# Optimization experiments

Measured on AMD Instinct MI355X. Metric: run time of the kernel, lower is better.

The kernel has to match this reference:

```python
import jax, jax.numpy as jnp
import numpy as np

SCALE = 2
GROUPS = 4
IN_CH = 256


def _init_pos(scale, groups):
    # torch: arange((-s+1)/2, (s-1)/2 + 1) / s
    h = (np.arange(scale) - (scale - 1) / 2.0) / scale
    hh, ww = np.meshgrid(h, h, indexing='ij')          # (s,s) each
    t = np.stack([hh, ww]).transpose(0, 2, 1)          # (2,s,s), transpose(1,2)
    rep = np.tile(t, (1, groups, 1))                   # (2, g*s, s)
    return jnp.asarray(rep.reshape(1, -1, 1, 1), dtype=jnp.float32)  # (1, 2*g*s^2, 1, 1)


def _pixel_shuffle(x, r):
    B, C, H, W = x.shape
    Co = C // (r * r)
    x = x.reshape(B, Co, r, r, H, W)
    x = x.transpose(0, 1, 4, 2, 5, 3)                  # (B,Co,H,r,W,r)
    return x.reshape(B, Co, H * r, W * r)


def _grid_sample_border(x, grid):
    # x: (N,C,H,W), grid: (N,Ho,Wo,2) in [-1,1], align_corners=False, border padding
    N, C, H, W = x.shape
    gx, gy = grid[..., 0], grid[..., 1]
    ix = jnp.clip(((gx + 1.0) * W - 1.0) * 0.5, 0.0, W - 1.0)
    iy = jnp.clip(((gy + 1.0) * H - 1.0) * 0.5, 0.0, H - 1.0)
    ix0 = jnp.floor(ix)
    iy0 = jnp.floor(iy)
    wx = (ix - ix0)[..., None]
    wy = (iy - iy0)[..., None]
    x0 = ix0.astype(jnp.int32)
    y0 = iy0.astype(jnp.int32)
    x1 = jnp.minimum(x0 + 1, W - 1)
    y1 = jnp.minimum(y0 + 1, H - 1)
    xt = x.transpose(0, 2, 3, 1)                       # NHWC for channel-last gather
    b = jnp.arange(N)[:, None, None]
    v00 = xt[b, y0, x0]
    v01 = xt[b, y0, x1]
    v10 = xt[b, y1, x0]
    v11 = xt[b, y1, x1]
    out = (v00 * (1 - wy) * (1 - wx) + v01 * (1 - wy) * wx
           + v10 * wy * (1 - wx) + v11 * wy * wx)      # (N,Ho,Wo,C)
    return out.transpose(0, 3, 1, 2)


def setup_inputs() -> dict:
    key = jax.random.key(0)
    k1, k2 = jax.random.split(key)
    B, C, H, W = 8, IN_CH, 80, 80
    out_ch = 2 * GROUPS * SCALE ** 2
    x = jax.random.normal(k1, (B, C, H, W), dtype=jnp.float32)
    w_off = jax.random.normal(k2, (out_ch, C, 1, 1), dtype=jnp.float32) * 0.001
    b_off = jnp.zeros((out_ch,), dtype=jnp.float32)
    return {"x": x, "w_off": w_off, "b_off": b_off}


def reference(x, w_off, b_off):
    B, C, H, W = x.shape
    s, g = SCALE, GROUPS
    # 1x1 conv predicting offsets
    off = jnp.einsum('bchw,oc->bohw', x, w_off[:, :, 0, 0]) + b_off[None, :, None, None]
    offset = off * 0.25 + _init_pos(s, g)              # (B, 2*g*s^2, H, W)
    offset = offset.reshape(B, 2, g * s * s, H, W)
    # pixel-center base coords: channel 0 = x (w), channel 1 = y (h)
    cx = jnp.arange(W, dtype=x.dtype) + 0.5
    cy = jnp.arange(H, dtype=x.dtype) + 0.5
    coords = jnp.stack([jnp.broadcast_to(cx[None, :], (H, W)),
                        jnp.broadcast_to(cy[:, None], (H, W))])   # (2,H,W)
    coords = coords[None, :, None]                     # (1,2,1,H,W)
    norm = jnp.array([W, H], dtype=x.dtype).reshape(1, 2, 1, 1, 1)
    coords = 2.0 * (coords + offset) / norm - 1.0      # (B,2,g*s^2,H,W)
    coords = coords.reshape(B, 2 * g * s * s, H, W)
    coords = _pixel_shuffle(coords, s)                 # (B, 2*g, s*H, s*W)
    coords = coords.reshape(B, 2, g, s * H, s * W)
    coords = coords.transpose(0, 2, 3, 4, 1).reshape(B * g, s * H, s * W, 2)
    xr = x.reshape(B * g, C // g, H, W)
    out = _grid_sample_border(xr, coords)              # (B*g, C/g, sH, sW)
    return out.reshape(B, C, s * H, s * W)
```

## Files before the change

kernel.cpp:

```cpp
#include <hip/hip_runtime.h>

#define W_IN 80
#define H_IN 80
#define HW_IN (W_IN * H_IN)
#define C_IN 256
#define NG 4
#define NOFF 32
#define W_OUT 160
#define H_OUT 160
#define HW_OUT (W_OUT * H_OUT)

__global__ __launch_bounds__(256) void conv_coords_kernel(
    const float* __restrict__ x, const float* __restrict__ w,
    const float* __restrict__ bias, float2* __restrict__ coords) {
  __shared__ float ws[C_IN * NOFF];
  const int t = threadIdx.x;
#pragma unroll
  for (int i = 0; i < (C_IN * NOFF) / 256; ++i) {
    int idx = i * 256 + t;
    int c = idx >> 5, o = idx & 31;
    ws[idx] = w[o * C_IN + c];
  }
  __syncthreads();

  const int p = blockIdx.x * 256 + t;
  const int b = p / HW_IN;
  const int yx = p - b * HW_IN;
  const float* xp = x + (size_t)b * C_IN * HW_IN + yx;

  float acc[NOFF];
#pragma unroll
  for (int o = 0; o < NOFF; ++o) acc[o] = bias[o];

#pragma unroll 4
  for (int c = 0; c < C_IN; ++c) {
    float v = xp[(size_t)c * HW_IN];
    const float4* w4 = reinterpret_cast<const float4*>(&ws[c * NOFF]);
#pragma unroll
    for (int o4 = 0; o4 < NOFF / 4; ++o4) {
      float4 wv = w4[o4];
      acc[o4 * 4 + 0] = fmaf(v, wv.x, acc[o4 * 4 + 0]);
      acc[o4 * 4 + 1] = fmaf(v, wv.y, acc[o4 * 4 + 1]);
      acc[o4 * 4 + 2] = fmaf(v, wv.z, acc[o4 * 4 + 2]);
      acc[o4 * 4 + 3] = fmaf(v, wv.w, acc[o4 * 4 + 3]);
    }
  }

  const int y = yx / W_IN;
  const int xc = yx - y * W_IN;
#pragma unroll
  for (int k = 0; k < 16; ++k) {
    float hx = (k & 1) ? 0.25f : -0.25f;
    float hy = (k & 2) ? 0.25f : -0.25f;
    float ix = fminf(fmaxf((float)xc + fmaf(0.25f, acc[k], hx), 0.0f),
                     (float)(W_IN - 1));
    float iy = fminf(fmaxf((float)y + fmaf(0.25f, acc[16 + k], hy), 0.0f),
                     (float)(H_IN - 1));
    coords[(size_t)(b * 16 + k) * HW_IN + yx] = make_float2(ix, iy);
  }
}

__global__ __launch_bounds__(256) void sample_kernel(
    const float* __restrict__ x, const float2* __restrict__ coords,
    float* __restrict__ out) {
  const int idx = blockIdx.x * 256 + threadIdx.x;
  const int ox = idx % W_OUT;
  const int r1d = idx / W_OUT;
  const int oy = r1d % H_OUT;
  const int r2d = r1d / H_OUT;
  const int gi = r2d & 3;
  const int b = r2d >> 2;

  const int xs = ox >> 1, j = ox & 1;
  const int ys = oy >> 1, i = oy & 1;
  const int k = gi * 4 + i * 2 + j;

  const float2 c2 = coords[(size_t)(b * 16 + k) * HW_IN + ys * W_IN + xs];
  const float fx0 = floorf(c2.x), fy0 = floorf(c2.y);
  const int x0 = (int)fx0, y0 = (int)fy0;
  const float wx = c2.x - fx0, wy = c2.y - fy0;
  const int x1 = min(x0 + 1, W_IN - 1), y1 = min(y0 + 1, H_IN - 1);

  const float w00 = (1.0f - wy) * (1.0f - wx);
  const float w01 = (1.0f - wy) * wx;
  const float w10 = wy * (1.0f - wx);
  const float w11 = wy * wx;

  const int o00 = y0 * W_IN + x0;
  const int o01 = y0 * W_IN + x1;
  const int o10 = y1 * W_IN + x0;
  const int o11 = y1 * W_IN + x1;

  const float* xp = x + (size_t)(b * C_IN + gi * 64) * HW_IN;
  float* op = out + (size_t)(b * C_IN + gi * 64) * HW_OUT + oy * W_OUT + ox;

#pragma unroll 4
  for (int c = 0; c < 64; ++c) {
    const float* pc = xp + c * HW_IN;
    float v = pc[o00] * w00 + pc[o01] * w01 + pc[o10] * w10 + pc[o11] * w11;
    op[c * HW_OUT] = v;
  }
}

extern "C" void kernel_launch(void* const* d_in, const int* in_sizes, int n_in,
                              void* d_out, int out_size, void* d_ws,
                              size_t ws_size, hipStream_t stream) {
  const float* x = (const float*)d_in[0];
  const float* w_off = (const float*)d_in[1];
  const float* b_off = (const float*)d_in[2];
  float* out = (float*)d_out;
  float2* coords = (float2*)d_ws;

  conv_coords_kernel<<<200, 256, 0, stream>>>(x, w_off, b_off, coords);
  sample_kernel<<<3200, 256, 0, stream>>>(x, coords, out);
}
```

Before: 329.2 us.

## Split conv channel reduction across waves and vectorize bilinear gathers

```diff
diff --git a/kernel.cpp b/kernel.cpp
--- a/kernel.cpp
+++ b/kernel.cpp
@@ -2,19 +2,24 @@
 
 #define W_IN 80
 #define H_IN 80
-#define HW_IN (W_IN * H_IN)
+#define HW_IN 6400
 #define C_IN 256
-#define NG 4
 #define NOFF 32
 #define W_OUT 160
 #define H_OUT 160
-#define HW_OUT (W_OUT * H_OUT)
+#define HW_OUT 25600
+
+typedef float f2u __attribute__((ext_vector_type(2), aligned(4)));
 
 __global__ __launch_bounds__(256) void conv_coords_kernel(
     const float* __restrict__ x, const float* __restrict__ w,
     const float* __restrict__ bias, float2* __restrict__ coords) {
   __shared__ float ws[C_IN * NOFF];
+  __shared__ float offb[64][NOFF + 1];
   const int t = threadIdx.x;
+  const int lane = t & 63;
+  const int wv = t >> 6;
+
 #pragma unroll
   for (int i = 0; i < (C_IN * NOFF) / 256; ++i) {
     int idx = i * 256 + t;
@@ -23,40 +28,70 @@
   }
   __syncthreads();
 
-  const int p = blockIdx.x * 256 + t;
-  const int b = p / HW_IN;
-  const int yx = p - b * HW_IN;
-  const float* xp = x + (size_t)b * C_IN * HW_IN + yx;
+  const int pix0 = blockIdx.x * 64;
+  const int b = blockIdx.x / 100;
+  const int yx0 = pix0 - b * HW_IN;
+  const int yx = yx0 + lane;
+
+  const float* xp = x + ((size_t)b * C_IN + wv * 64) * HW_IN + yx;
 
   float acc[NOFF];
 #pragma unroll
-  for (int o = 0; o < NOFF; ++o) acc[o] = bias[o];
+  for (int o = 0; o < NOFF; ++o) acc[o] = 0.0f;
 
 #pragma unroll 4
-  for (int c = 0; c < C_IN; ++c) {
-    float v = xp[(size_t)c * HW_IN];
-    const float4* w4 = reinterpret_cast<const float4*>(&ws[c * NOFF]);
+  for (int cc = 0; cc < 64; ++cc) {
+    float v = xp[(size_t)cc * HW_IN];
+    const float4* w4 = reinterpret_cast<const float4*>(&ws[(wv * 64 + cc) * NOFF]);
 #pragma unroll
     for (int o4 = 0; o4 < NOFF / 4; ++o4) {
-      float4 wv = w4[o4];
-      acc[o4 * 4 + 0] = fmaf(v, wv.x, acc[o4 * 4 + 0]);
-      acc[o4 * 4 + 1] = fmaf(v, wv.y, acc[o4 * 4 + 1]);
-      acc[o4 * 4 + 2] = fmaf(v, wv.z, acc[o4 * 4 + 2]);
-      acc[o4 * 4 + 3] = fmaf(v, wv.w, acc[o4 * 4 + 3]);
+      float4 wvv = w4[o4];
+      acc[o4 * 4 + 0] = fmaf(v, wvv.x, acc[o4 * 4 + 0]);
+      acc[o4 * 4 + 1] = fmaf(v, wvv.y, acc[o4 * 4 + 1]);
+      acc[o4 * 4 + 2] = fmaf(v, wvv.z, acc[o4 * 4 + 2]);
+      acc[o4 * 4 + 3] = fmaf(v, wvv.w, acc[o4 * 4 + 3]);
     }
   }
 
-  const int y = yx / W_IN;
-  const int xc = yx - y * W_IN;
+  __syncthreads();
+  if (wv == 0) {
 #pragma unroll
-  for (int k = 0; k < 16; ++k) {
+    for (int o = 0; o < NOFF; ++o) offb[lane][o] = acc[o] + bias[o];
+  }
+  __syncthreads();
+  if (wv == 1) {
+#pragma unroll
+    for (int o = 0; o < NOFF; ++o) offb[lane][o] += acc[o];
+  }
+  __syncthreads();
+  if (wv == 2) {
+#pragma unroll
+    for (int o = 0; o < NOFF; ++o) offb[lane][o] += acc[o];
+  }
+  __syncthreads();
+  if (wv == 3) {
+#pragma unroll
+    for (int o = 0; o < NOFF; ++o) offb[lane][o] += acc[o];
+  }
+  __syncthreads();
+
+#pragma unroll
+  for (int r = 0; r < 4; ++r) {
+    int id = r * 256 + t;
+    int k = id >> 6;
+    int px = id & 63;
+    float offx = offb[px][k];
+    float offy = offb[px][16 + k];
+    int yxp = yx0 + px;
+    int y = yxp / W_IN;
+    int xc = yxp - y * W_IN;
     float hx = (k & 1) ? 0.25f : -0.25f;
     float hy = (k & 2) ? 0.25f : -0.25f;
-    float ix = fminf(fmaxf((float)xc + fmaf(0.25f, acc[k], hx), 0.0f),
+    float ix = fminf(fmaxf((float)xc + fmaf(0.25f, offx, hx), 0.0f),
                      (float)(W_IN - 1));
-    float iy = fminf(fmaxf((float)y + fmaf(0.25f, acc[16 + k], hy), 0.0f),
+    float iy = fminf(fmaxf((float)y + fmaf(0.25f, offy, hy), 0.0f),
                      (float)(H_IN - 1));
-    coords[(size_t)(b * 16 + k) * HW_IN + yx] = make_float2(ix, iy);
+    coords[((size_t)b * 16 + k) * HW_IN + yxp] = make_float2(ix, iy);
   }
 }
 
@@ -65,40 +100,41 @@
     float* __restrict__ out) {
   const int idx = blockIdx.x * 256 + threadIdx.x;
   const int ox = idx % W_OUT;
-  const int r1d = idx / W_OUT;
-  const int oy = r1d % H_OUT;
-  const int r2d = r1d / H_OUT;
-  const int gi = r2d & 3;
-  const int b = r2d >> 2;
+  const int r1 = idx / W_OUT;
+  const int oy = r1 % H_OUT;
+  const int r2 = r1 / H_OUT;
+  const int gi = r2 & 3;
+  const int b = r2 >> 2;
 
   const int xs = ox >> 1, j = ox & 1;
   const int ys = oy >> 1, i = oy & 1;
   const int k = gi * 4 + i * 2 + j;
 
-  const float2 c2 = coords[(size_t)(b * 16 + k) * HW_IN + ys * W_IN + xs];
+  const float2 c2 = coords[((size_t)b * 16 + k) * HW_IN + ys * W_IN + xs];
   const float fx0 = floorf(c2.x), fy0 = floorf(c2.y);
   const int x0 = (int)fx0, y0 = (int)fy0;
   const float wx = c2.x - fx0, wy = c2.y - fy0;
-  const int x1 = min(x0 + 1, W_IN - 1), y1 = min(y0 + 1, H_IN - 1);
+  const int y1 = min(y0 + 1, H_IN - 1);
+  const int xl = min(x0, W_IN - 2);
+  const bool xe = (x0 == W_IN - 1);
 
-  const float w00 = (1.0f - wy) * (1.0f - wx);
-  const float w01 = (1.0f - wy) * wx;
-  const float w10 = wy * (1.0f - wx);
-  const float w11 = wy * wx;
+  const int o0 = y0 * W_IN + xl;
+  const int o1 = y1 * W_IN + xl;
 
-  const int o00 = y0 * W_IN + x0;
-  const int o01 = y0 * W_IN + x1;
-  const int o10 = y1 * W_IN + x0;
-  const int o11 = y1 * W_IN + x1;
-
-  const float* xp = x + (size_t)(b * C_IN + gi * 64) * HW_IN;
-  float* op = out + (size_t)(b * C_IN + gi * 64) * HW_OUT + oy * W_OUT + ox;
+  const float* xp = x + ((size_t)b * C_IN + gi * 64) * HW_IN;
+  float* op = out + ((size_t)b * C_IN + gi * 64) * HW_OUT + oy * W_OUT + ox;
 
 #pragma unroll 4
   for (int c = 0; c < 64; ++c) {
     const float* pc = xp + c * HW_IN;
-    float v = pc[o00] * w00 + pc[o01] * w01 + pc[o10] * w10 + pc[o11] * w11;
-    op[c * HW_OUT] = v;
+    f2u a = *reinterpret_cast<const f2u*>(pc + o0);
+    f2u bt = *reinterpret_cast<const f2u*>(pc + o1);
+    float v00 = xe ? a.y : a.x;
+    float v10 = xe ? bt.y : bt.x;
+    float h0 = fmaf(wx, a.y - v00, v00);
+    float h1 = fmaf(wx, bt.y - v10, v10);
+    float v = fmaf(wy, h1 - h0, h0);
+    __builtin_nontemporal_store(v, &op[(size_t)c * HW_OUT]);
   }
 }
 
@@ -111,6 +147,6 @@
   float* out = (float*)d_out;
   float2* coords = (float2*)d_ws;
 
-  conv_coords_kernel<<<200, 256, 0, stream>>>(x, w_off, b_off, coords);
+  conv_coords_kernel<<<800, 256, 0, stream>>>(x, w_off, b_off, coords);
   sample_kernel<<<3200, 256, 0, stream>>>(x, coords, out);
 }
```

After: 299.4 us. -9.0%, faster.
